# Kernel optimization log

Hardware: AMD Instinct MI355X
Metric: run time of the kernel (lower is better)

## Reference

```python
import jax, jax.numpy as jnp
import numpy as np

EMBED_DIM = 1024
NUM_HEADS = 16
HEAD_DIM = EMBED_DIM // NUM_HEADS


def setup_inputs() -> dict:
    key = jax.random.key(0)
    ks = jax.random.split(key, 9)
    B, S, E, Hd = 1, 4096, EMBED_DIM, HEAD_DIM
    s = 0.02
    return {
        "x": jax.random.normal(ks[0], (B, S, E), jnp.float32),
        "mask": jnp.ones((B, S, S), jnp.int32),
        "Wq": jax.random.normal(ks[1], (E, E), jnp.float32) * s,
        "bq": jnp.zeros((E,), jnp.float32),
        "Wk": jax.random.normal(ks[2], (E, Hd), jnp.float32) * s,
        "bk": jnp.zeros((Hd,), jnp.float32),
        "Wv": jax.random.normal(ks[3], (E, Hd), jnp.float32) * s,
        "bv": jnp.zeros((Hd,), jnp.float32),
        "Wo": jax.random.normal(ks[4], (E, E), jnp.float32) * s,
        "bo": jnp.zeros((E,), jnp.float32),
    }


def reference(x, mask, Wq, bq, Wk, bk, Wv, bv, Wo, bo):
    B, S, E = x.shape
    H, Hd = NUM_HEADS, HEAD_DIM
    q = (x @ Wq + bq).reshape(B, S, H, Hd).transpose(0, 2, 1, 3)  # [B,H,S,Hd]
    k = x @ Wk + bk  # [B,S,Hd] single KV head (MQA)
    v = x @ Wv + bv  # [B,S,Hd]
    scale = 1.0 / np.sqrt(Hd).astype(np.float32)
    # broadcast single-head K across all query heads
    qk = jnp.einsum('bhqd,bkd->bhqk', q, k) * scale  # [B,H,S,S]
    qk = jnp.where(mask[:, None, :, :] == 0, jnp.float32(-10000.0), qk)
    attn = jax.nn.softmax(qk, axis=-1)
    out = jnp.einsum('bhqk,bkd->bhqd', attn, v)  # [B,H,S,Hd]
    out = out.transpose(0, 2, 1, 3).reshape(B, S, E)
    return out @ Wo + bo
```

## Files before the change

kernel.cpp:

```cpp
#include <hip/hip_runtime.h>
#include <hip/hip_bf16.h>
#include <stdint.h>

typedef __bf16 bf16x8 __attribute__((ext_vector_type(8)));
typedef float f32x4 __attribute__((ext_vector_type(4)));
typedef float f32x16 __attribute__((ext_vector_type(16)));
typedef unsigned int uint2v __attribute__((ext_vector_type(2)));

#define E_DIM 1024
#define HD 64
#define NH 16
#define QKV_LD 1152
#define LOG2E 1.44269504088896f

__device__ __forceinline__ float toF(float x) { return x; }
__device__ __forceinline__ float toF(__hip_bfloat16 x) { return __bfloat162float(x); }
__device__ __forceinline__ void storeOut(float* p, float v) { *p = v; }
__device__ __forceinline__ void storeOut(__hip_bfloat16* p, float v) { *p = __float2bfloat16(v); }

__device__ __forceinline__ unsigned cvtpk_bf16(float lo, float hi_) {
    unsigned r;
    asm("v_cvt_pk_bf16_f32 %0, %1, %2" : "=v"(r) : "v"(lo), "v"(hi_));
    return r;
}
__device__ __forceinline__ void perm32swap(unsigned& a, unsigned& b) {
    uint2v r = __builtin_amdgcn_permlane32_swap(a, b, false, false);
    a = r.x; b = r.y;
}
__device__ __forceinline__ float fexp2(float x) {
    float r;
    asm("v_exp_f32 %0, %1" : "=v"(r) : "v"(x));
    return r;
}

typedef __attribute__((address_space(1))) void gvoid;
typedef __attribute__((address_space(3))) void lvoid;
__device__ __forceinline__ void gload_lds16(const void* g, void* l) {
    __builtin_amdgcn_global_load_lds((gvoid*)g, (lvoid*)l, 16, 0, 0);
}

__global__ void cast_f32_bf16_kernel(const float* __restrict__ in, __hip_bfloat16* __restrict__ o, int n) {
    int i = (blockIdx.x * blockDim.x + threadIdx.x) * 4;
    if (i + 3 < n) {
        float4 v = *reinterpret_cast<const float4*>(in + i);
        __hip_bfloat16 t[4] = {__float2bfloat16(v.x), __float2bfloat16(v.y),
                               __float2bfloat16(v.z), __float2bfloat16(v.w)};
        *reinterpret_cast<uint2*>(o + i) = *reinterpret_cast<uint2*>(t);
    }
}

template<typename InT>
__global__ void transpose_cast_kernel(const InT* __restrict__ in, int ldi,
                                      __hip_bfloat16* __restrict__ out, int ldo,
                                      int R, int C) {
    __shared__ float tile[32][33];
    const int bx = blockIdx.x * 32;
    const int by = blockIdx.y * 32;
    const int tx = threadIdx.x & 31, ty = threadIdx.x >> 5;
#pragma unroll
    for (int j = 0; j < 4; ++j) {
        int r = bx + ty + j * 8, c = by + tx;
        tile[ty + j * 8][tx] = toF(in[(size_t)r * ldi + c]);
    }
    __syncthreads();
#pragma unroll
    for (int j = 0; j < 4; ++j) {
        int c = by + ty + j * 8, r = bx + tx;
        out[(size_t)c * ldo + r] = __float2bfloat16(tile[tx][ty + j * 8]);
    }
}

__global__ void concat_bias3_kernel(const float* __restrict__ bq, const float* __restrict__ bk,
                                    const float* __restrict__ bv, float* __restrict__ bqkv) {
    int i = blockIdx.x * blockDim.x + threadIdx.x;
    if (i < E_DIM) bqkv[i] = bq[i];
    else if (i < E_DIM + HD) bqkv[i] = bk[i - E_DIM];
    else if (i < E_DIM + 2 * HD) bqkv[i] = bv[i - E_DIM - HD];
}

__global__ void maskbits_kernel(const int* __restrict__ mask, unsigned long long* __restrict__ mb,
                                int nwords) {
    int gtid = blockIdx.x * blockDim.x + threadIdx.x;
    int wid = gtid >> 6, lane = gtid & 63;
    int nw = (gridDim.x * blockDim.x) >> 6;
    for (int w = wid; w < nwords; w += nw) {
        int v = mask[(size_t)w * 64 + lane];
        unsigned long long b = __ballot(v != 0);
        if (lane == 0) mb[w] = b;
    }
}

template<typename OutT>
__global__ __launch_bounds__(256)
void gemm_bt2_kernel(const __hip_bfloat16* __restrict__ A,
                     const __hip_bfloat16* __restrict__ Bt,
                     const float* __restrict__ bias,
                     OutT* __restrict__ C,
                     int M, int N, int K, float sQ, int nQ, float sKV) {
    constexpr int BM = 128, BN = 128, BK = 64;
    __shared__ __align__(16) unsigned char lA[2][BM * BK * 2];
    __shared__ __align__(16) unsigned char lB[2][BN * BK * 2];
    const int ntn = N / BN;
    const int tm = blockIdx.x / ntn, tn = blockIdx.x % ntn;
    const int tid = threadIdx.x, lane = tid & 63, wave = tid >> 6;
    const int l15 = lane & 15, l4 = lane >> 4;
    const int wm = (wave >> 1) * 64, wn = (wave & 1) * 64;
    const int r0 = tm * BM, c0 = tn * BN;
    const int NK = K / BK;

    size_t aoff[4], boff[4];
    unsigned ldso[4];
#pragma unroll
    for (int i = 0; i < 4; ++i) {
        int row = wave * 32 + i * 8 + (lane >> 3);
        int c = (lane & 7) ^ (row & 7);
        aoff[i] = (size_t)(r0 + row) * K * 2 + c * 16;
        boff[i] = (size_t)(c0 + row) * K * 2 + c * 16;
        ldso[i] = wave * 4096 + i * 1024;
    }
    const char* Ab = (const char*)A;
    const char* Bb = (const char*)Bt;

#pragma unroll
    for (int i = 0; i < 4; ++i) {
        gload_lds16(Ab + aoff[i], &lA[0][ldso[i]]);
        gload_lds16(Bb + boff[i], &lB[0][ldso[i]]);
    }
    __syncthreads();

    f32x4 z4 = {0.f, 0.f, 0.f, 0.f};
    f32x4 acc[4][4];
#pragma unroll
    for (int mi = 0; mi < 4; ++mi)
#pragma unroll
        for (int ni = 0; ni < 4; ++ni) acc[mi][ni] = z4;

    int buf = 0;
    for (int ks = 0; ks < NK; ++ks) {
        if (ks + 1 < NK) {
            size_t kb = (size_t)(ks + 1) * BK * 2;
#pragma unroll
            for (int i = 0; i < 4; ++i) {
                gload_lds16(Ab + aoff[i] + kb, &lA[buf ^ 1][ldso[i]]);
                gload_lds16(Bb + boff[i] + kb, &lB[buf ^ 1][ldso[i]]);
            }
        }
        bf16x8 af[4][2], bf[4][2];
#pragma unroll
        for (int mi = 0; mi < 4; ++mi) {
            int row = wm + mi * 16 + l15;
#pragma unroll
            for (int kh = 0; kh < 2; ++kh) {
                int slot = (kh * 4 + l4) ^ (row & 7);
                af[mi][kh] = *reinterpret_cast<const bf16x8*>(&lA[buf][row * 128 + slot * 16]);
            }
        }
#pragma unroll
        for (int ni = 0; ni < 4; ++ni) {
            int row = wn + ni * 16 + l15;
#pragma unroll
            for (int kh = 0; kh < 2; ++kh) {
                int slot = (kh * 4 + l4) ^ (row & 7);
                bf[ni][kh] = *reinterpret_cast<const bf16x8*>(&lB[buf][row * 128 + slot * 16]);
            }
        }
        __builtin_amdgcn_s_setprio(1);
#pragma unroll
        for (int mi = 0; mi < 4; ++mi)
#pragma unroll
            for (int ni = 0; ni < 4; ++ni) {
                acc[mi][ni] = __builtin_amdgcn_mfma_f32_16x16x32_bf16(af[mi][0], bf[ni][0], acc[mi][ni], 0, 0, 0);
                acc[mi][ni] = __builtin_amdgcn_mfma_f32_16x16x32_bf16(af[mi][1], bf[ni][1], acc[mi][ni], 0, 0, 0);
            }
        __builtin_amdgcn_s_setprio(0);
        __syncthreads();
        buf ^= 1;
    }

#pragma unroll
    for (int ni = 0; ni < 4; ++ni) {
        int col = c0 + wn + ni * 16 + l15;
        float b = bias[col];
        float s = (col < nQ) ? sQ : sKV;
#pragma unroll
        for (int mi = 0; mi < 4; ++mi) {
            int row = r0 + wm + mi * 16 + l4 * 4;
#pragma unroll
            for (int r = 0; r < 4; ++r) {
                float v = (acc[mi][ni][r] + b) * s;
                storeOut(C + (size_t)(row + r) * N + col, v);
            }
        }
    }
}

__global__ __launch_bounds__(256, 2)
void mqa5_kernel(const __hip_bfloat16* __restrict__ qkv,
                 const __hip_bfloat16* __restrict__ vtb,
                 const unsigned long long* __restrict__ mbits,
                 __hip_bfloat16* __restrict__ attnb,
                 int S) {
    __shared__ __align__(16) unsigned char sKV[2][32768];
    const int tid = threadIdx.x, lane = tid & 63, w = tid >> 6;
    const int r31 = lane & 31, hi = lane >> 5, rx = r31 & 15;
    const int q0 = blockIdx.x * 32;
    const int h = blockIdx.y * 4 + w;
    const int NT = S / 128, NW64 = S / 64;
    const __hip_bfloat16* kvb = qkv + E_DIM;

    bf16x8 qf[4];
    {
        const __hip_bfloat16* qp = qkv + (size_t)(q0 + r31) * QKV_LD + h * HD + hi * 8;
#pragma unroll
        for (int s = 0; s < 4; ++s) qf[s] = *reinterpret_cast<const bf16x8*>(qp + 16 * s);
    }

    const char* gbase[8];
    int gstep[8];
    unsigned ldsoff[8];
#pragma unroll
    for (int i = 0; i < 8; ++i) {
        int r = w * 32 + i * 4 + (lane >> 4);
        int sl = lane & 15;
        int c = sl ^ (r & 15);
        if (c < 8) {
            gbase[i] = (const char*)(kvb + (size_t)r * QKV_LD + c * 8);
            gstep[i] = 128 * QKV_LD * 2;
        } else {
            gbase[i] = (const char*)(vtb + (size_t)(r & 63) * S + (r >> 6) * 64 + (c - 8) * 8);
            gstep[i] = 128 * 2;
        }
        ldsoff[i] = w * 8192 + i * 1024;
    }

#pragma unroll
    for (int i = 0; i < 8; ++i) { gload_lds16(gbase[i], &sKV[0][ldsoff[i]]); gbase[i] += gstep[i]; }
    __syncthreads();

    float rm = -3e38f, rl = 0.f;
    f32x16 oacc[2];
#pragma unroll
    for (int i = 0; i < 16; ++i) { oacc[0][i] = 0.f; oacc[1][i] = 0.f; }

    int buf = 0;
    for (int t = 0; t < NT; ++t) {
        if (t + 1 < NT) {
#pragma unroll
            for (int i = 0; i < 8; ++i) { gload_lds16(gbase[i], &sKV[buf ^ 1][ldsoff[i]]); gbase[i] += gstep[i]; }
        }
        ulonglong2 wb = *reinterpret_cast<const ulonglong2*>(
            mbits + (size_t)(q0 + r31) * NW64 + 2 * t);
        const unsigned char* bp = sKV[buf];

        f32x16 sacc[4];
        __builtin_amdgcn_s_setprio(1);
#pragma unroll
        for (int kb = 0; kb < 4; ++kb) {
            const unsigned char* rowp = bp + (kb * 32 + r31) * 256;
            f32x16 a;
#pragma unroll
            for (int i = 0; i < 16; ++i) a[i] = 0.f;
#pragma unroll
            for (int s = 0; s < 4; ++s) {
                int slot = (2 * s + hi) ^ rx;
                bf16x8 kf = *reinterpret_cast<const bf16x8*>(rowp + slot * 16);
                a = __builtin_amdgcn_mfma_f32_32x32x16_bf16(kf, qf[s], a, 0, 0, 0);
            }
            sacc[kb] = a;
        }
        __builtin_amdgcn_s_setprio(0);

        if ((wb.x & wb.y) != ~0ull) {
#pragma unroll
            for (int kb = 0; kb < 4; ++kb) {
                unsigned long long wv = (kb < 2) ? wb.x : wb.y;
                int base = (kb & 1) * 32;
#pragma unroll
                for (int r = 0; r < 16; ++r) {
                    int kl = base + (r & 3) + 8 * (r >> 2) + 4 * hi;
                    if (!((wv >> kl) & 1)) sacc[kb][r] = -14427.0f;
                }
            }
        }

        float t0[8];
#pragma unroll
        for (int j = 0; j < 8; ++j) {
            float a01 = fmaxf(fmaxf(sacc[0][j], sacc[0][j + 8]), fmaxf(sacc[1][j], sacc[1][j + 8]));
            float a23 = fmaxf(fmaxf(sacc[2][j], sacc[2][j + 8]), fmaxf(sacc[3][j], sacc[3][j + 8]));
            t0[j] = fmaxf(a01, a23);
        }
        float u0 = fmaxf(t0[0], t0[4]), u1 = fmaxf(t0[1], t0[5]);
        float u2 = fmaxf(t0[2], t0[6]), u3 = fmaxf(t0[3], t0[7]);
        float pmax = fmaxf(fmaxf(u0, u1), fmaxf(u2, u3));
        pmax = fmaxf(pmax, __shfl_xor(pmax, 32));

        if (!__all(pmax - rm <= 8.0f)) {
            float rmn = fmaxf(rm, pmax);
            float al = fexp2(rm - rmn);
            rl *= al;
#pragma unroll
            for (int r = 0; r < 16; ++r) { oacc[0][r] *= al; oacc[1][r] *= al; }
            rm = rmn;
        }

        float s0 = 0.f, s1 = 0.f, s2 = 0.f, s3 = 0.f;
#pragma unroll
        for (int kb = 0; kb < 4; ++kb) {
#pragma unroll
            for (int r = 0; r < 16; r += 4) {
                sacc[kb][r + 0] = fexp2(sacc[kb][r + 0] - rm); s0 += sacc[kb][r + 0];
                sacc[kb][r + 1] = fexp2(sacc[kb][r + 1] - rm); s1 += sacc[kb][r + 1];
                sacc[kb][r + 2] = fexp2(sacc[kb][r + 2] - rm); s2 += sacc[kb][r + 2];
                sacc[kb][r + 3] = fexp2(sacc[kb][r + 3] - rm); s3 += sacc[kb][r + 3];
            }
        }
        float sum = (s0 + s1) + (s2 + s3);
        sum += __shfl_xor(sum, 32);
        rl += sum;

        bf16x8 pa[8];
#pragma unroll
        for (int kb = 0; kb < 4; ++kb) {
#pragma unroll
            for (int half = 0; half < 2; ++half) {
                int b0 = half * 8;
                unsigned A = cvtpk_bf16(sacc[kb][b0 + 0], sacc[kb][b0 + 1]);
                unsigned B = cvtpk_bf16(sacc[kb][b0 + 2], sacc[kb][b0 + 3]);
                unsigned C = cvtpk_bf16(sacc[kb][b0 + 4], sacc[kb][b0 + 5]);
                unsigned D = cvtpk_bf16(sacc[kb][b0 + 6], sacc[kb][b0 + 7]);
                perm32swap(A, C);
                perm32swap(B, D);
                union { unsigned u[4]; bf16x8 v; } pk;
                pk.u[0] = A; pk.u[1] = B; pk.u[2] = C; pk.u[3] = D;
                pa[kb * 2 + half] = pk.v;
            }
        }

        __builtin_amdgcn_s_setprio(1);
#pragma unroll
        for (int db = 0; db < 2; ++db) {
            f32x16 a = oacc[db];
#pragma unroll
            for (int j = 0; j < 2; ++j) {
                const unsigned char* rowp = bp + (j * 64 + db * 32 + r31) * 256;
#pragma unroll
                for (int s = 0; s < 4; ++s) {
                    int slot = (8 + 2 * s + hi) ^ rx;
                    bf16x8 vf = *reinterpret_cast<const bf16x8*>(rowp + slot * 16);
                    a = __builtin_amdgcn_mfma_f32_32x32x16_bf16(vf, pa[j * 4 + s], a, 0, 0, 0);
                }
            }
            oacc[db] = a;
        }
        __builtin_amdgcn_s_setprio(0);

        __syncthreads();
        buf ^= 1;
    }

    float inv = 1.0f / rl;
    __hip_bfloat16* op = attnb + (size_t)(q0 + r31) * E_DIM + h * HD;
#pragma unroll
    for (int db = 0; db < 2; ++db)
#pragma unroll
        for (int m = 0; m < 4; ++m) {
            uint2 pk;
            pk.x = cvtpk_bf16(oacc[db][4 * m + 0] * inv, oacc[db][4 * m + 1] * inv);
            pk.y = cvtpk_bf16(oacc[db][4 * m + 2] * inv, oacc[db][4 * m + 3] * inv);
            *reinterpret_cast<uint2*>(op + db * 32 + m * 8 + hi * 4) = pk;
        }
}

extern "C" void kernel_launch(void* const* d_in, const int* in_sizes, int n_in,
                              void* d_out, int out_size, void* d_ws, size_t ws_size,
                              hipStream_t stream) {
    (void)n_in; (void)out_size; (void)ws_size;
    const float* x  = (const float*)d_in[0];
    const int* mask = (const int*)d_in[1];
    const float* Wq = (const float*)d_in[2];
    const float* bq = (const float*)d_in[3];
    const float* Wk = (const float*)d_in[4];
    const float* bk = (const float*)d_in[5];
    const float* Wv = (const float*)d_in[6];
    const float* bv = (const float*)d_in[7];
    const float* Wo = (const float*)d_in[8];
    const float* bo = (const float*)d_in[9];
    float* out = (float*)d_out;

    const int E = E_DIM;
    const int S = in_sizes[0] / E;

    char* ws = (char*)d_ws;
    size_t off = 0;
    auto alloc = [&](size_t b) { char* p = ws + off; off += (b + 255) & ~(size_t)255; return p; };
    __hip_bfloat16* xb     = (__hip_bfloat16*)alloc((size_t)S * E * 2);
    __hip_bfloat16* wqkvT  = (__hip_bfloat16*)alloc((size_t)QKV_LD * E * 2);
    __hip_bfloat16* woT    = (__hip_bfloat16*)alloc((size_t)E * E * 2);
    __hip_bfloat16* qkvb   = (__hip_bfloat16*)alloc((size_t)S * QKV_LD * 2);
    __hip_bfloat16* vtb    = (__hip_bfloat16*)alloc((size_t)HD * S * 2);
    __hip_bfloat16* attnb  = (__hip_bfloat16*)alloc((size_t)S * E * 2);
    float* bqkv  = (float*)alloc(QKV_LD * 4);
    unsigned long long* mbits = (unsigned long long*)alloc((size_t)S * (S / 64) * 8);

    cast_f32_bf16_kernel<<<dim3((S * E / 4 + 255) / 256), dim3(256), 0, stream>>>(x, xb, S * E);
    transpose_cast_kernel<float><<<dim3(E / 32, E / 32), dim3(256), 0, stream>>>(Wq, E, wqkvT, E, E, E);
    transpose_cast_kernel<float><<<dim3(E / 32, HD / 32), dim3(256), 0, stream>>>(
        Wk, HD, wqkvT + (size_t)E * E, E, E, HD);
    transpose_cast_kernel<float><<<dim3(E / 32, HD / 32), dim3(256), 0, stream>>>(
        Wv, HD, wqkvT + (size_t)(E + HD) * E, E, E, HD);
    transpose_cast_kernel<float><<<dim3(E / 32, E / 32), dim3(256), 0, stream>>>(Wo, E, woT, E, E, E);
    concat_bias3_kernel<<<dim3((QKV_LD + 255) / 256), dim3(256), 0, stream>>>(bq, bk, bv, bqkv);
    maskbits_kernel<<<dim3(1024), dim3(256), 0, stream>>>(mask, mbits, S * (S / 64));

    gemm_bt2_kernel<__hip_bfloat16><<<dim3((S / 128) * (QKV_LD / 128)), dim3(256), 0, stream>>>(
        xb, wqkvT, bqkv, qkvb, S, QKV_LD, E, 0.125f * LOG2E, E, 1.0f);
    transpose_cast_kernel<__hip_bfloat16><<<dim3(S / 32, HD / 32), dim3(256), 0, stream>>>(
        qkvb + E + HD, QKV_LD, vtb, S, S, HD);
    mqa5_kernel<<<dim3(S / 32, NH / 4), dim3(256), 0, stream>>>(qkvb, vtb, mbits, attnb, S);
    gemm_bt2_kernel<float><<<dim3((S / 128) * (E / 128)), dim3(256), 0, stream>>>(
        attnb, woT, bo, out, S, E, E, 1.0f, E, 1.0f);
}
```

Measured before the change: 181.1 us.

## Software-pipeline MQA attention with split K/V buffers and MFMA row sums

Splits the shared K/V buffer into separate double-buffered K and V tiles and restructures the attention loop so the QK^T for the next tile is computed while softmax and PV run on the current one, unrolled by two. Row sums of the softmax probabilities are computed with an extra MFMA against a vector of ones instead of VALU adds plus a cross-lane shuffle. The four weight transpose launches are merged into one grid launch. This aims to overlap matrix work with the exp/softmax VALU work and cut launch overhead, at the cost of more registers (two score sets live) and extra MFMA issue slots.

New measurement: 253.4 us. 1.4x slower.

```diff
diff --git a/kernel.cpp b/kernel.cpp
--- a/kernel.cpp
+++ b/kernel.cpp
@@ -67,6 +67,35 @@
     for (int j = 0; j < 4; ++j) {
         int c = by + ty + j * 8, r = bx + tx;
         out[(size_t)c * ldo + r] = __float2bfloat16(tile[tx][ty + j * 8]);
+    }
+}
+
+__global__ __launch_bounds__(256)
+void transpose4_kernel(const float* __restrict__ Wq, const float* __restrict__ Wk,
+                       const float* __restrict__ Wv, const float* __restrict__ Wo,
+                       __hip_bfloat16* __restrict__ wqkvT, __hip_bfloat16* __restrict__ woT) {
+    const int z = blockIdx.z;
+    const float* in; __hip_bfloat16* out; int ldi;
+    if (z == 0)      { in = Wq; out = wqkvT;                                ldi = E_DIM; }
+    else if (z == 1) { if (blockIdx.y >= HD / 32) return;
+                       in = Wk; out = wqkvT + (size_t)E_DIM * E_DIM;        ldi = HD; }
+    else if (z == 2) { if (blockIdx.y >= HD / 32) return;
+                       in = Wv; out = wqkvT + (size_t)(E_DIM + HD) * E_DIM; ldi = HD; }
+    else             { in = Wo; out = woT;                                  ldi = E_DIM; }
+    __shared__ float tile[32][33];
+    const int bx = blockIdx.x * 32;
+    const int by = blockIdx.y * 32;
+    const int tx = threadIdx.x & 31, ty = threadIdx.x >> 5;
+#pragma unroll
+    for (int j = 0; j < 4; ++j) {
+        int r = bx + ty + j * 8, c = by + tx;
+        tile[ty + j * 8][tx] = in[(size_t)r * ldi + c];
+    }
+    __syncthreads();
+#pragma unroll
+    for (int j = 0; j < 4; ++j) {
+        int c = by + ty + j * 8, r = bx + tx;
+        out[(size_t)c * E_DIM + r] = __float2bfloat16(tile[tx][ty + j * 8]);
     }
 }
 
@@ -194,19 +223,123 @@
     }
 }
 
+
+__device__ __forceinline__ void qkt_f(const unsigned char* __restrict__ kb,
+                                      const bf16x8 (&qf)[4], f32x16 (&sacc)[4],
+                                      int r31, int hi) {
+    const int swz = r31 & 7;
+    f32x16 z;
+#pragma unroll
+    for (int i = 0; i < 16; ++i) z[i] = 0.f;
+    __builtin_amdgcn_s_setprio(1);
+#pragma unroll
+    for (int b = 0; b < 4; ++b) {
+        const unsigned char* rowp = kb + (b * 32 + r31) * 128;
+        f32x16 a = z;
+#pragma unroll
+        for (int s = 0; s < 4; ++s) {
+            int slot = (2 * s + hi) ^ swz;
+            bf16x8 kf = *reinterpret_cast<const bf16x8*>(rowp + slot * 16);
+            a = __builtin_amdgcn_mfma_f32_32x32x16_bf16(kf, qf[s], a, 0, 0, 0);
+        }
+        sacc[b] = a;
+    }
+    __builtin_amdgcn_s_setprio(0);
+}
+
+__device__ __forceinline__ void smpv_f(f32x16 (&sacc)[4], const unsigned char* __restrict__ vb,
+                                       ulonglong2 wb, float& rm, f32x16 (&oacc)[2],
+                                       f32x16& lacc, const bf16x8& ones,
+                                       int r31, int hi) {
+    if ((wb.x & wb.y) != ~0ull) {
+#pragma unroll
+        for (int b = 0; b < 4; ++b) {
+            unsigned long long wv = (b < 2) ? wb.x : wb.y;
+            int base = (b & 1) * 32;
+#pragma unroll
+            for (int r = 0; r < 16; ++r) {
+                int kl = base + (r & 3) + 8 * (r >> 2) + 4 * hi;
+                if (!((wv >> kl) & 1)) sacc[b][r] = -14427.0f;
+            }
+        }
+    }
+    float t0[8];
+#pragma unroll
+    for (int j = 0; j < 8; ++j) {
+        float a01 = fmaxf(fmaxf(sacc[0][j], sacc[0][j + 8]), fmaxf(sacc[1][j], sacc[1][j + 8]));
+        float a23 = fmaxf(fmaxf(sacc[2][j], sacc[2][j + 8]), fmaxf(sacc[3][j], sacc[3][j + 8]));
+        t0[j] = fmaxf(a01, a23);
+    }
+    float u0 = fmaxf(fmaxf(t0[0], t0[4]), fmaxf(t0[1], t0[5]));
+    float u1 = fmaxf(fmaxf(t0[2], t0[6]), fmaxf(t0[3], t0[7]));
+    float pmax = fmaxf(u0, u1);
+    if (!__all(pmax - rm <= 8.0f)) {
+        float pm2 = fmaxf(pmax, __shfl_xor(pmax, 32));
+        float rmn = fmaxf(rm, pm2);
+        float al = fexp2(rm - rmn);
+#pragma unroll
+        for (int r = 0; r < 16; ++r) { oacc[0][r] *= al; oacc[1][r] *= al; lacc[r] *= al; }
+        rm = rmn;
+    }
+#pragma unroll
+    for (int b = 0; b < 4; ++b)
+#pragma unroll
+        for (int r = 0; r < 16; ++r) sacc[b][r] = fexp2(sacc[b][r] - rm);
+    bf16x8 pa[8];
+#pragma unroll
+    for (int b = 0; b < 4; ++b) {
+#pragma unroll
+        for (int half = 0; half < 2; ++half) {
+            int b0 = half * 8;
+            unsigned A = cvtpk_bf16(sacc[b][b0 + 0], sacc[b][b0 + 1]);
+            unsigned B = cvtpk_bf16(sacc[b][b0 + 2], sacc[b][b0 + 3]);
+            unsigned C = cvtpk_bf16(sacc[b][b0 + 4], sacc[b][b0 + 5]);
+            unsigned D = cvtpk_bf16(sacc[b][b0 + 6], sacc[b][b0 + 7]);
+            perm32swap(A, C);
+            perm32swap(B, D);
+            union { unsigned u[4]; bf16x8 v; } pk;
+            pk.u[0] = A; pk.u[1] = B; pk.u[2] = C; pk.u[3] = D;
+            pa[b * 2 + half] = pk.v;
+        }
+    }
+    const int swz = r31 & 7;
+    __builtin_amdgcn_s_setprio(1);
+#pragma unroll
+    for (int db = 0; db < 2; ++db) {
+        f32x16 a = oacc[db];
+#pragma unroll
+        for (int j = 0; j < 2; ++j) {
+            const unsigned char* rowp = vb + (j * 64 + db * 32 + r31) * 128;
+#pragma unroll
+            for (int s = 0; s < 4; ++s) {
+                int slot = (2 * s + hi) ^ swz;
+                bf16x8 vf = *reinterpret_cast<const bf16x8*>(rowp + slot * 16);
+                a = __builtin_amdgcn_mfma_f32_32x32x16_bf16(vf, pa[j * 4 + s], a, 0, 0, 0);
+            }
+        }
+        oacc[db] = a;
+    }
+#pragma unroll
+    for (int u = 0; u < 8; ++u)
+        lacc = __builtin_amdgcn_mfma_f32_32x32x16_bf16(ones, pa[u], lacc, 0, 0, 0);
+    __builtin_amdgcn_s_setprio(0);
+}
+
 __global__ __launch_bounds__(256, 2)
-void mqa5_kernel(const __hip_bfloat16* __restrict__ qkv,
+void mqa6_kernel(const __hip_bfloat16* __restrict__ qkv,
                  const __hip_bfloat16* __restrict__ vtb,
                  const unsigned long long* __restrict__ mbits,
                  __hip_bfloat16* __restrict__ attnb,
                  int S) {
-    __shared__ __align__(16) unsigned char sKV[2][32768];
+    __shared__ __align__(16) unsigned char Kb[2][16384];
+    __shared__ __align__(16) unsigned char Vb[2][16384];
     const int tid = threadIdx.x, lane = tid & 63, w = tid >> 6;
-    const int r31 = lane & 31, hi = lane >> 5, rx = r31 & 15;
+    const int r31 = lane & 31, hi = lane >> 5;
     const int q0 = blockIdx.x * 32;
     const int h = blockIdx.y * 4 + w;
     const int NT = S / 128, NW64 = S / 64;
-    const __hip_bfloat16* kvb = qkv + E_DIM;
+    const char* kvb = (const char*)(qkv + E_DIM);
+    const char* vtc = (const char*)vtb;
 
     bf16x8 qf[4];
     {
@@ -214,152 +347,76 @@
 #pragma unroll
         for (int s = 0; s < 4; ++s) qf[s] = *reinterpret_cast<const bf16x8*>(qp + 16 * s);
     }
-
-    const char* gbase[8];
-    int gstep[8];
-    unsigned ldsoff[8];
-#pragma unroll
-    for (int i = 0; i < 8; ++i) {
-        int r = w * 32 + i * 4 + (lane >> 4);
-        int sl = lane & 15;
-        int c = sl ^ (r & 15);
-        if (c < 8) {
-            gbase[i] = (const char*)(kvb + (size_t)r * QKV_LD + c * 8);
-            gstep[i] = 128 * QKV_LD * 2;
-        } else {
-            gbase[i] = (const char*)(vtb + (size_t)(r & 63) * S + (r >> 6) * 64 + (c - 8) * 8);
-            gstep[i] = 128 * 2;
-        }
-        ldsoff[i] = w * 8192 + i * 1024;
-    }
-
-#pragma unroll
-    for (int i = 0; i < 8; ++i) { gload_lds16(gbase[i], &sKV[0][ldsoff[i]]); gbase[i] += gstep[i]; }
+    bf16x8 ones;
+#pragma unroll
+    for (int i = 0; i < 8; ++i) ones[i] = (__bf16)1.0f;
+
+    unsigned kOff[4], vOff[4], lOff[4];
+#pragma unroll
+    for (int i = 0; i < 4; ++i) {
+        int row = w * 32 + i * 8 + (lane >> 3);
+        int c = (lane & 7) ^ (row & 7);
+        kOff[i] = (unsigned)(row * QKV_LD * 2 + c * 16);
+        vOff[i] = (unsigned)(((row & 63) * S + (row >> 6) * 64 + c * 8) * 2);
+        lOff[i] = (unsigned)(w * 4096 + i * 1024);
+    }
+    const unsigned STEPK = 128u * QKV_LD * 2u;
+    const unsigned STEPV = 256u;
+
+#pragma unroll
+    for (int i = 0; i < 4; ++i) gload_lds16(kvb + kOff[i], &Kb[0][lOff[i]]);
+#pragma unroll
+    for (int i = 0; i < 4; ++i) gload_lds16(kvb + kOff[i] + STEPK, &Kb[1][lOff[i]]);
+#pragma unroll
+    for (int i = 0; i < 4; ++i) gload_lds16(vtc + vOff[i], &Vb[0][lOff[i]]);
     __syncthreads();
 
-    float rm = -3e38f, rl = 0.f;
-    f32x16 oacc[2];
-#pragma unroll
-    for (int i = 0; i < 16; ++i) { oacc[0][i] = 0.f; oacc[1][i] = 0.f; }
-
-    int buf = 0;
-    for (int t = 0; t < NT; ++t) {
-        if (t + 1 < NT) {
-#pragma unroll
-            for (int i = 0; i < 8; ++i) { gload_lds16(gbase[i], &sKV[buf ^ 1][ldsoff[i]]); gbase[i] += gstep[i]; }
-        }
-        ulonglong2 wb = *reinterpret_cast<const ulonglong2*>(
-            mbits + (size_t)(q0 + r31) * NW64 + 2 * t);
-        const unsigned char* bp = sKV[buf];
-
-        f32x16 sacc[4];
-        __builtin_amdgcn_s_setprio(1);
-#pragma unroll
-        for (int kb = 0; kb < 4; ++kb) {
-            const unsigned char* rowp = bp + (kb * 32 + r31) * 256;
-            f32x16 a;
-#pragma unroll
-            for (int i = 0; i < 16; ++i) a[i] = 0.f;
-#pragma unroll
-            for (int s = 0; s < 4; ++s) {
-                int slot = (2 * s + hi) ^ rx;
-                bf16x8 kf = *reinterpret_cast<const bf16x8*>(rowp + slot * 16);
-                a = __builtin_amdgcn_mfma_f32_32x32x16_bf16(kf, qf[s], a, 0, 0, 0);
-            }
-            sacc[kb] = a;
-        }
-        __builtin_amdgcn_s_setprio(0);
-
-        if ((wb.x & wb.y) != ~0ull) {
-#pragma unroll
-            for (int kb = 0; kb < 4; ++kb) {
-                unsigned long long wv = (kb < 2) ? wb.x : wb.y;
-                int base = (kb & 1) * 32;
-#pragma unroll
-                for (int r = 0; r < 16; ++r) {
-                    int kl = base + (r & 3) + 8 * (r >> 2) + 4 * hi;
-                    if (!((wv >> kl) & 1)) sacc[kb][r] = -14427.0f;
-                }
-            }
-        }
-
-        float t0[8];
-#pragma unroll
-        for (int j = 0; j < 8; ++j) {
-            float a01 = fmaxf(fmaxf(sacc[0][j], sacc[0][j + 8]), fmaxf(sacc[1][j], sacc[1][j + 8]));
-            float a23 = fmaxf(fmaxf(sacc[2][j], sacc[2][j + 8]), fmaxf(sacc[3][j], sacc[3][j + 8]));
-            t0[j] = fmaxf(a01, a23);
-        }
-        float u0 = fmaxf(t0[0], t0[4]), u1 = fmaxf(t0[1], t0[5]);
-        float u2 = fmaxf(t0[2], t0[6]), u3 = fmaxf(t0[3], t0[7]);
-        float pmax = fmaxf(fmaxf(u0, u1), fmaxf(u2, u3));
-        pmax = fmaxf(pmax, __shfl_xor(pmax, 32));
-
-        if (!__all(pmax - rm <= 8.0f)) {
-            float rmn = fmaxf(rm, pmax);
-            float al = fexp2(rm - rmn);
-            rl *= al;
-#pragma unroll
-            for (int r = 0; r < 16; ++r) { oacc[0][r] *= al; oacc[1][r] *= al; }
-            rm = rmn;
-        }
-
-        float s0 = 0.f, s1 = 0.f, s2 = 0.f, s3 = 0.f;
-#pragma unroll
-        for (int kb = 0; kb < 4; ++kb) {
-#pragma unroll
-            for (int r = 0; r < 16; r += 4) {
-                sacc[kb][r + 0] = fexp2(sacc[kb][r + 0] - rm); s0 += sacc[kb][r + 0];
-                sacc[kb][r + 1] = fexp2(sacc[kb][r + 1] - rm); s1 += sacc[kb][r + 1];
-                sacc[kb][r + 2] = fexp2(sacc[kb][r + 2] - rm); s2 += sacc[kb][r + 2];
-                sacc[kb][r + 3] = fexp2(sacc[kb][r + 3] - rm); s3 += sacc[kb][r + 3];
-            }
-        }
-        float sum = (s0 + s1) + (s2 + s3);
-        sum += __shfl_xor(sum, 32);
-        rl += sum;
-
-        bf16x8 pa[8];
-#pragma unroll
-        for (int kb = 0; kb < 4; ++kb) {
-#pragma unroll
-            for (int half = 0; half < 2; ++half) {
-                int b0 = half * 8;
-                unsigned A = cvtpk_bf16(sacc[kb][b0 + 0], sacc[kb][b0 + 1]);
-                unsigned B = cvtpk_bf16(sacc[kb][b0 + 2], sacc[kb][b0 + 3]);
-                unsigned C = cvtpk_bf16(sacc[kb][b0 + 4], sacc[kb][b0 + 5]);
-                unsigned D = cvtpk_bf16(sacc[kb][b0 + 6], sacc[kb][b0 + 7]);
-                perm32swap(A, C);
-                perm32swap(B, D);
-                union { unsigned u[4]; bf16x8 v; } pk;
-                pk.u[0] = A; pk.u[1] = B; pk.u[2] = C; pk.u[3] = D;
-                pa[kb * 2 + half] = pk.v;
-            }
-        }
-
-        __builtin_amdgcn_s_setprio(1);
-#pragma unroll
-        for (int db = 0; db < 2; ++db) {
-            f32x16 a = oacc[db];
-#pragma unroll
-            for (int j = 0; j < 2; ++j) {
-                const unsigned char* rowp = bp + (j * 64 + db * 32 + r31) * 256;
-#pragma unroll
-                for (int s = 0; s < 4; ++s) {
-                    int slot = (8 + 2 * s + hi) ^ rx;
-                    bf16x8 vf = *reinterpret_cast<const bf16x8*>(rowp + slot * 16);
-                    a = __builtin_amdgcn_mfma_f32_32x32x16_bf16(vf, pa[j * 4 + s], a, 0, 0, 0);
-                }
-            }
-            oacc[db] = a;
-        }
-        __builtin_amdgcn_s_setprio(0);
-
-        __syncthreads();
-        buf ^= 1;
-    }
-
-    float inv = 1.0f / rl;
+    float rm = -3e38f;
+    f32x16 oacc[2], lacc;
+#pragma unroll
+    for (int i = 0; i < 16; ++i) { oacc[0][i] = 0.f; oacc[1][i] = 0.f; lacc[i] = 0.f; }
+    f32x16 sA[4], sB[4];
+    qkt_f(Kb[0], qf, sA, r31, hi);
+
+    const size_t mrow = (size_t)(q0 + r31) * NW64;
+    for (int tt = 0; tt < NT / 2; ++tt) {
+        {
+            const int t = 2 * tt;
+            ulonglong2 wb = *reinterpret_cast<const ulonglong2*>(mbits + mrow + 2 * t);
+            if (t + 2 < NT) {
+                unsigned ko = (unsigned)(t + 2) * STEPK;
+#pragma unroll
+                for (int i = 0; i < 4; ++i) gload_lds16(kvb + kOff[i] + ko, &Kb[0][lOff[i]]);
+            }
+            if (t + 1 < NT) {
+                unsigned vo = (unsigned)(t + 1) * STEPV;
+#pragma unroll
+                for (int i = 0; i < 4; ++i) gload_lds16(vtc + vOff[i] + vo, &Vb[1][lOff[i]]);
+                qkt_f(Kb[1], qf, sB, r31, hi);
+            }
+            smpv_f(sA, Vb[0], wb, rm, oacc, lacc, ones, r31, hi);
+            __syncthreads();
+        }
+        {
+            const int t = 2 * tt + 1;
+            ulonglong2 wb = *reinterpret_cast<const ulonglong2*>(mbits + mrow + 2 * t);
+            if (t + 2 < NT) {
+                unsigned ko = (unsigned)(t + 2) * STEPK;
+#pragma unroll
+                for (int i = 0; i < 4; ++i) gload_lds16(kvb + kOff[i] + ko, &Kb[1][lOff[i]]);
+            }
+            if (t + 1 < NT) {
+                unsigned vo = (unsigned)(t + 1) * STEPV;
+#pragma unroll
+                for (int i = 0; i < 4; ++i) gload_lds16(vtc + vOff[i] + vo, &Vb[0][lOff[i]]);
+                qkt_f(Kb[0], qf, sA, r31, hi);
+            }
+            smpv_f(sB, Vb[1], wb, rm, oacc, lacc, ones, r31, hi);
+            __syncthreads();
+        }
+    }
+
+    float inv = 1.0f / lacc[0];
     __hip_bfloat16* op = attnb + (size_t)(q0 + r31) * E_DIM + h * HD;
 #pragma unroll
     for (int db = 0; db < 2; ++db)
@@ -404,12 +461,7 @@
     unsigned long long* mbits = (unsigned long long*)alloc((size_t)S * (S / 64) * 8);
 
     cast_f32_bf16_kernel<<<dim3((S * E / 4 + 255) / 256), dim3(256), 0, stream>>>(x, xb, S * E);
-    transpose_cast_kernel<float><<<dim3(E / 32, E / 32), dim3(256), 0, stream>>>(Wq, E, wqkvT, E, E, E);
-    transpose_cast_kernel<float><<<dim3(E / 32, HD / 32), dim3(256), 0, stream>>>(
-        Wk, HD, wqkvT + (size_t)E * E, E, E, HD);
-    transpose_cast_kernel<float><<<dim3(E / 32, HD / 32), dim3(256), 0, stream>>>(
-        Wv, HD, wqkvT + (size_t)(E + HD) * E, E, E, HD);
-    transpose_cast_kernel<float><<<dim3(E / 32, E / 32), dim3(256), 0, stream>>>(Wo, E, woT, E, E, E);
+    transpose4_kernel<<<dim3(E / 32, E / 32, 4), dim3(256), 0, stream>>>(Wq, Wk, Wv, Wo, wqkvT, woT);
     concat_bias3_kernel<<<dim3((QKV_LD + 255) / 256), dim3(256), 0, stream>>>(bq, bk, bv, bqkv);
     maskbits_kernel<<<dim3(1024), dim3(256), 0, stream>>>(mask, mbits, S * (S / 64));
 
@@ -417,7 +469,7 @@
         xb, wqkvT, bqkv, qkvb, S, QKV_LD, E, 0.125f * LOG2E, E, 1.0f);
     transpose_cast_kernel<__hip_bfloat16><<<dim3(S / 32, HD / 32), dim3(256), 0, stream>>>(
         qkvb + E + HD, QKV_LD, vtb, S, S, HD);
-    mqa5_kernel<<<dim3(S / 32, NH / 4), dim3(256), 0, stream>>>(qkvb, vtb, mbits, attnb, S);
+    mqa6_kernel<<<dim3(S / 32, NH / 4), dim3(256), 0, stream>>>(qkvb, vtb, mbits, attnb, S);
     gemm_bt2_kernel<float><<<dim3((S / 128) * (E / 128)), dim3(256), 0, stream>>>(
         attnb, woT, bo, out, S, E, E, 1.0f, E, 1.0f);
 }
```
